# Kernel tuning notes

Measured on AMD Instinct MI355X. Metric: run time of the kernel, lower is better.

The kernel has to match this reference:

```python
import jax, jax.numpy as jnp
import numpy as np

EMBED = 1024
HEADS = 16

def setup_inputs() -> dict:
    key = jax.random.key(0)
    ks = jax.random.split(key, 6)
    N, S = 1, 4096
    half = EMBED // 2
    x = jax.random.normal(ks[0], (N, S, EMBED), dtype=jnp.float32)
    Wq = jax.random.normal(ks[1], (half, half), dtype=jnp.float32) * 0.02
    Wk = jax.random.normal(ks[2], (half, half), dtype=jnp.float32) * 0.02
    Wv = jax.random.normal(ks[3], (half, half), dtype=jnp.float32) * 0.02
    Wo = jax.random.normal(ks[4], (EMBED, half), dtype=jnp.float32) * 0.02
    bo = jnp.zeros((EMBED,), dtype=jnp.float32)
    return {"x": x, "Wq": Wq, "Wk": Wk, "Wv": Wv, "Wo": Wo, "bo": bo}

def reference(x, Wq, Wk, Wv, Wo, bo):
    N, S, E = x.shape
    H = HEADS
    Dh = (E // 2) // H                 # per-head dim of the half-width projections (32)
    scale = float(E // H) ** 0.5       # original scales by head_dim = embed/heads = 64
    left = x[..., : E // 2]            # only the left chunk feeds attention in the source
    # torch Linear: y = x @ W.T (no bias)
    q = (left @ Wq.T).reshape(N, S, H, Dh)
    k = (left @ Wk.T).reshape(N, S, H, Dh)
    v = (left @ Wv.T).reshape(N, S, H, Dh)
    energy = jnp.einsum('nqhd,nkhd->nqkh', q, k)          # [N,S,S,H] full score tensor
    att = jax.nn.softmax(energy / scale, axis=2)          # softmax over key axis
    out = jnp.einsum('nqkh,nkhd->nqhd', att, v)           # [N,S,H,Dh]
    out = out.reshape(N, S, E // 2)
    return out @ Wo.T + bo                                # fc_out: half -> embed
```

## Files before the change

kernel.cpp:

```cpp
#include <hip/hip_runtime.h>
#include <stdint.h>


#define SEQ    4096
#define DMODEL 1024
#define DHALF  512
#define NH     16
#define DH     32

typedef __attribute__((ext_vector_type(4))) float facc4;
typedef __attribute__((ext_vector_type(8))) short bfrag8;

#define MFMA_BF16(a, b, c) __builtin_amdgcn_mfma_f32_16x16x32_bf16((a), (b), (c), 0, 0, 0)

static __device__ __forceinline__ uint16_t f2b(float x) {
    uint32_t u = __float_as_uint(x);
    return (uint16_t)((u + 0x7FFFu + ((u >> 16) & 1u)) >> 16);
}
static __device__ __forceinline__ float b2f(uint16_t b) {
    return __uint_as_float(((uint32_t)b) << 16);
}

static __device__ __forceinline__ bfrag8 cvt8perm(float4 a, float4 b) {
    uint32_t u0 = __float_as_uint(a.x) + 0x8000u, u1 = __float_as_uint(a.y) + 0x8000u;
    uint32_t u2 = __float_as_uint(a.z) + 0x8000u, u3 = __float_as_uint(a.w) + 0x8000u;
    uint32_t u4 = __float_as_uint(b.x) + 0x8000u, u5 = __float_as_uint(b.y) + 0x8000u;
    uint32_t u6 = __float_as_uint(b.z) + 0x8000u, u7 = __float_as_uint(b.w) + 0x8000u;
    union { uint32_t w[4]; bfrag8 r; } u;
    u.w[0] = __builtin_amdgcn_perm(u1, u0, 0x07060302u);
    u.w[1] = __builtin_amdgcn_perm(u3, u2, 0x07060302u);
    u.w[2] = __builtin_amdgcn_perm(u5, u4, 0x07060302u);
    u.w[3] = __builtin_amdgcn_perm(u7, u6, 0x07060302u);
    return u.r;
}

__global__ __launch_bounds__(256) void convert_w(
    const float* __restrict__ Wq, const float* __restrict__ Wk,
    const float* __restrict__ Wv, const float* __restrict__ Wo,
    const float* __restrict__ x,
    uint16_t* __restrict__ q, uint16_t* __restrict__ k,
    uint16_t* __restrict__ v, uint16_t* __restrict__ o,
    uint16_t* __restrict__ xb)
{
    int zz = blockIdx.x;
    if (zz >= 640) {
        size_t g = (size_t)(zz - 640) * 2048 + (size_t)threadIdx.x * 8;
        int row = (int)(g >> 9);
        int col = (int)(g & 511);
        const float* src = &x[(size_t)row * DMODEL + col];
        float4 a = *(const float4*)src;
        float4 b = *(const float4*)(src + 4);
        *(bfrag8*)&xb[g] = cvt8perm(a, b);
        return;
    }
    const float* src; uint16_t* dst; size_t off;
    if      (zz < 128) { src = Wq; dst = q; off = (size_t)zz * 2048; }
    else if (zz < 256) { src = Wk; dst = k; off = (size_t)(zz - 128) * 2048; }
    else if (zz < 384) { src = Wv; dst = v; off = (size_t)(zz - 256) * 2048; }
    else               { src = Wo; dst = o; off = (size_t)(zz - 384) * 2048; }
    size_t i = off + (size_t)threadIdx.x * 8;
    float4 a = *(const float4*)&src[i];
    float4 b = *(const float4*)&src[i + 4];
    *(bfrag8*)&dst[i] = cvt8perm(a, b);
}

__device__ __forceinline__ void gemm128(
    const uint16_t* __restrict__ A, int lda,
    const uint16_t* __restrict__ B, int ldb,
    void* __restrict__ C, int ldc, int cF32,
    const float* __restrict__ bias, float scale,
    int Kd, int m0, int n0)
{
    __shared__ __align__(16) uint16_t As[2][128 * 40];
    __shared__ __align__(16) uint16_t Bs[2][128 * 40];

    const int tid  = threadIdx.x;
    const int lane = tid & 63;
    const int wv   = tid >> 6;
    const int lo   = lane & 15;
    const int quad = lane >> 4;
    const int srow = tid >> 2;
    const int skq  = (tid & 3) * 8;
    const int rb   = (wv >> 1) * 64;
    const int cb   = (wv & 1) * 64;

    const facc4 ZACC = {0.f, 0.f, 0.f, 0.f};
    facc4 acc[4][4];
#pragma unroll
    for (int i = 0; i < 4; ++i)
#pragma unroll
        for (int j = 0; j < 4; ++j) acc[i][j] = ZACC;

    const uint16_t* hA0 = &A[(size_t)(m0 + srow) * lda + skq];
    const uint16_t* hA1 = &A[(size_t)(m0 + srow + 64) * lda + skq];
    const uint16_t* pB0 = &B[(size_t)(n0 + srow) * ldb + skq];
    const uint16_t* pB1 = &B[(size_t)(n0 + srow + 64) * ldb + skq];

    bfrag8 ra0 = *(const bfrag8*)hA0;
    bfrag8 ra1 = *(const bfrag8*)hA1;
    bfrag8 rb0 = *(const bfrag8*)pB0;
    bfrag8 rb1 = *(const bfrag8*)pB1;

    *(bfrag8*)&As[0][srow * 40 + skq]        = ra0;
    *(bfrag8*)&As[0][(srow + 64) * 40 + skq] = ra1;
    *(bfrag8*)&Bs[0][srow * 40 + skq]        = rb0;
    *(bfrag8*)&Bs[0][(srow + 64) * 40 + skq] = rb1;
    __syncthreads();

    int p = 0;
    for (int kt = 0; kt < Kd; kt += 32) {
        const bool more = (kt + 32 < Kd);
        if (more) {
            ra0 = *(const bfrag8*)(hA0 + kt + 32);
            ra1 = *(const bfrag8*)(hA1 + kt + 32);
            rb0 = *(const bfrag8*)(pB0 + kt + 32);
            rb1 = *(const bfrag8*)(pB1 + kt + 32);
        }

        bfrag8 af[4], bf[4];
#pragma unroll
        for (int i = 0; i < 4; ++i) {
            af[i] = *(const bfrag8*)&As[p][(rb + i * 16 + lo) * 40 + quad * 8];
            bf[i] = *(const bfrag8*)&Bs[p][(cb + i * 16 + lo) * 40 + quad * 8];
        }
#pragma unroll
        for (int i = 0; i < 4; ++i)
#pragma unroll
            for (int j = 0; j < 4; ++j)
                acc[i][j] = MFMA_BF16(bf[j], af[i], acc[i][j]);

        if (more) {
            *(bfrag8*)&As[1 - p][srow * 40 + skq]        = ra0;
            *(bfrag8*)&As[1 - p][(srow + 64) * 40 + skq] = ra1;
            *(bfrag8*)&Bs[1 - p][srow * 40 + skq]        = rb0;
            *(bfrag8*)&Bs[1 - p][(srow + 64) * 40 + skq] = rb1;
            __syncthreads();
            p ^= 1;
        }
    }

#pragma unroll
    for (int i = 0; i < 4; ++i) {
        const size_t row = (size_t)(m0 + rb + i * 16 + lo);
#pragma unroll
        for (int j = 0; j < 4; ++j) {
            const int colb = n0 + cb + j * 16 + quad * 4;
            float4 bv = {0.f, 0.f, 0.f, 0.f};
            if (bias) bv = *(const float4*)&bias[colb];
            float v0 = acc[i][j][0] * scale + bv.x;
            float v1 = acc[i][j][1] * scale + bv.y;
            float v2 = acc[i][j][2] * scale + bv.z;
            float v3 = acc[i][j][3] * scale + bv.w;
            if (cF32) {
                float4 o = {v0, v1, v2, v3};
                *(float4*)&((float*)C)[row * ldc + colb] = o;
            } else {
                uint2 o;
                o.x = (uint32_t)f2b(v0) | ((uint32_t)f2b(v1) << 16);
                o.y = (uint32_t)f2b(v2) | ((uint32_t)f2b(v3) << 16);
                *(uint2*)&((uint16_t*)C)[row * ldc + colb] = o;
            }
        }
    }
}

#define SC_Q (0.125f * 1.4426950408889634f)

__global__ __launch_bounds__(256, 2) void qkv_kernel(
    const uint16_t* __restrict__ xb,
    const uint16_t* __restrict__ Wqb, const uint16_t* __restrict__ Wkb,
    const uint16_t* __restrict__ Wvb,
    uint16_t* __restrict__ Q, uint16_t* __restrict__ K, uint16_t* __restrict__ V)
{
    const int z = blockIdx.z;
    const uint16_t* W = (z == 0) ? Wqb : (z == 1) ? Wkb : Wvb;
    uint16_t* Out     = (z == 0) ? Q   : (z == 1) ? K   : V;
    float scale       = (z == 0) ? SC_Q : 1.0f;
    gemm128(xb, DHALF, W, DHALF, Out, DHALF, 0, nullptr, scale, DHALF,
            blockIdx.y * 128, blockIdx.x * 128);
}

__global__ __launch_bounds__(256, 2) void outproj_kernel(
    const uint16_t* __restrict__ O, const uint16_t* __restrict__ Wob,
    const float* __restrict__ bo, float* __restrict__ Y)
{
    gemm128(O, DHALF, Wob, DHALF, Y, DMODEL, 1, bo, 1.0f, DHALF,
            blockIdx.y * 128, blockIdx.x * 128);
}

__global__ __launch_bounds__(512) void attn_kernel(
    const uint16_t* __restrict__ Q, const uint16_t* __restrict__ Kb,
    const uint16_t* __restrict__ Vb, uint16_t* __restrict__ Op,
    float* __restrict__ lbuf, int kspan)
{
    __shared__ __align__(16) uint16_t Ks[2][128 * 40];
    __shared__ __align__(16) uint16_t Vt[2][32 * 128];

    const int tid  = threadIdx.x;
    const int lane = tid & 63;
    const int wv   = tid >> 6;
    const int lo   = lane & 15;
    const int quad = lane >> 4;

    const int f  = blockIdx.x + 16 * blockIdx.y + 256 * blockIdx.z;
    const int pp = (f & 7) | ((f >> 7) << 3);
    const int h  = pp & 15;
    const int sp = pp >> 4;
    const int q0 = ((f >> 3) & 15) * 256;

    const int srow = tid >> 2;
    const int skq  = (tid & 3) * 8;

    const facc4 ZACC = {0.f, 0.f, 0.f, 0.f};

    bfrag8 qf[2];
    qf[0] = *(const bfrag8*)&Q[(size_t)(q0 + wv * 32 + lo) * DHALF + h * DH + quad * 8];
    qf[1] = *(const bfrag8*)&Q[(size_t)(q0 + wv * 32 + 16 + lo) * DHALF + h * DH + quad * 8];

    bfrag8 ones;
#pragma unroll
    for (int j = 0; j < 8; ++j) ones[j] = (short)0x3F80;

    int vt_w[8];
    {
        int pb = ((srow >> 5) << 2) | ((srow >> 2) & 3);
        int pw = (((srow >> 4) & 1) << 2) | (srow & 3);
#pragma unroll
        for (int j = 0; j < 8; ++j) {
            int d  = skq + j;
            int Rd = ((d & 7) + 2 * (d >> 3)) & 7;
            vt_w[j] = d * 128 + (((pb + Rd) & 15) << 3) + pw;
        }
    }
    int vt_r[4][2];
#pragma unroll
    for (int dt = 0; dt < 2; ++dt) {
        int d  = dt * 16 + lo;
        int Rd = ((d & 7) + 2 * (d >> 3)) & 7;
#pragma unroll
        for (int c = 0; c < 4; ++c)
            vt_r[c][dt] = d * 128 + ((((c * 4 + quad) + Rd) & 15) << 3);
    }
    const int ks_r = lo * 40 + quad * 8;

    const uint16_t* kp = &Kb[(size_t)(sp * kspan + srow) * DHALF + h * DH + skq];
    const uint16_t* vp = &Vb[(size_t)(sp * kspan + srow) * DHALF + h * DH + skq];

    facc4 oacc[2][2], oaccL[2];
    oacc[0][0] = ZACC; oacc[0][1] = ZACC;
    oacc[1][0] = ZACC; oacc[1][1] = ZACC;
    oaccL[0] = ZACC; oaccL[1] = ZACC;

    float4 kreg = *(const float4*)kp;
    float4 vreg = *(const float4*)vp;
    kp += 128 * DHALF;
    vp += 128 * DHALF;

#define STAGE(BUF) do {                                                       \
        *(float4*)&Ks[BUF][srow * 40 + skq] = kreg;                           \
        const uint16_t* vsp = (const uint16_t*)&vreg;                         \
        _Pragma("unroll")                                                     \
        for (int j = 0; j < 8; ++j) Vt[BUF][vt_w[j]] = vsp[j];                \
    } while (0)

#define HALF(BUF, HH) do {                                                    \
        uint2 w0[4], w1[4];                                                   \
        _Pragma("unroll")                                                     \
        for (int t4 = 0; t4 < 4; ++t4) {                                      \
            bfrag8 kf = *(const bfrag8*)&Ks[BUF][(4 * HH + t4) * 640 + ks_r]; \
            facc4 s0 = MFMA_BF16(kf, qf[0], ZACC);                            \
            facc4 s1 = MFMA_BF16(kf, qf[1], ZACC);                            \
            uint32_t a0 = __float_as_uint(__builtin_amdgcn_exp2f(s0[0])) + 0x8000u; \
            uint32_t a1 = __float_as_uint(__builtin_amdgcn_exp2f(s0[1])) + 0x8000u; \
            uint32_t a2 = __float_as_uint(__builtin_amdgcn_exp2f(s0[2])) + 0x8000u; \
            uint32_t a3 = __float_as_uint(__builtin_amdgcn_exp2f(s0[3])) + 0x8000u; \
            w0[t4].x = __builtin_amdgcn_perm(a1, a0, 0x07060302u);            \
            w0[t4].y = __builtin_amdgcn_perm(a3, a2, 0x07060302u);            \
            uint32_t b0 = __float_as_uint(__builtin_amdgcn_exp2f(s1[0])) + 0x8000u; \
            uint32_t b1 = __float_as_uint(__builtin_amdgcn_exp2f(s1[1])) + 0x8000u; \
            uint32_t b2 = __float_as_uint(__builtin_amdgcn_exp2f(s1[2])) + 0x8000u; \
            uint32_t b3 = __float_as_uint(__builtin_amdgcn_exp2f(s1[3])) + 0x8000u; \
            w1[t4].x = __builtin_amdgcn_perm(b1, b0, 0x07060302u);            \
            w1[t4].y = __builtin_amdgcn_perm(b3, b2, 0x07060302u);            \
        }                                                                     \
        union PU { uint2 u2[2]; bfrag8 f; } pu;                               \
        bfrag8 pf0[2], pf1[2];                                                \
        pu.u2[0] = w0[0]; pu.u2[1] = w0[1]; pf0[0] = pu.f;                    \
        pu.u2[0] = w0[2]; pu.u2[1] = w0[3]; pf0[1] = pu.f;                    \
        pu.u2[0] = w1[0]; pu.u2[1] = w1[1]; pf1[0] = pu.f;                    \
        pu.u2[0] = w1[2]; pu.u2[1] = w1[3]; pf1[1] = pu.f;                    \
        _Pragma("unroll")                                                     \
        for (int cc = 0; cc < 2; ++cc) {                                      \
            _Pragma("unroll")                                                 \
            for (int dt = 0; dt < 2; ++dt) {                                  \
                bfrag8 vf = *(const bfrag8*)&Vt[BUF][vt_r[2 * HH + cc][dt]];  \
                oacc[0][dt] = MFMA_BF16(pf0[cc], vf, oacc[0][dt]);            \
                oacc[1][dt] = MFMA_BF16(pf1[cc], vf, oacc[1][dt]);            \
            }                                                                 \
            oaccL[0] = MFMA_BF16(pf0[cc], ones, oaccL[0]);                    \
            oaccL[1] = MFMA_BF16(pf1[cc], ones, oaccL[1]);                    \
        }                                                                     \
    } while (0)

#define TILE(BUF) do { HALF(BUF, 0); HALF(BUF, 1); } while (0)

    STAGE(0);
    __syncthreads();

    const int nt = kspan >> 7;
    for (int t = 0; t < nt; t += 2) {
        kreg = *(const float4*)kp;
        vreg = *(const float4*)vp;
        kp += 128 * DHALF; vp += 128 * DHALF;
        TILE(0);
        STAGE(1);
        __syncthreads();

        const bool more = (t + 2 < nt);
        if (more) {
            kreg = *(const float4*)kp;
            vreg = *(const float4*)vp;
            kp += 128 * DHALF; vp += 128 * DHALF;
        }
        TILE(1);
        if (more) {
            STAGE(0);
            __syncthreads();
        }
    }
#undef STAGE
#undef HALF
#undef TILE

    if (lo == 0) {
#pragma unroll
        for (int g = 0; g < 2; ++g)
#pragma unroll
            for (int r = 0; r < 4; ++r)
                lbuf[((size_t)sp * NH + h) * SEQ + q0 + wv * 32 + g * 16 + quad * 4 + r] =
                    oaccL[g][r];
    }

    uint16_t* Od = Op + (size_t)sp * SEQ * DHALF;
#pragma unroll
    for (int g = 0; g < 2; ++g) {
#pragma unroll
        for (int r = 0; r < 4; ++r) {
            int row = q0 + wv * 32 + g * 16 + quad * 4 + r;
            Od[(size_t)row * DHALF + h * DH + lo]      = f2b(oacc[g][0][r]);
            Od[(size_t)row * DHALF + h * DH + 16 + lo] = f2b(oacc[g][1][r]);
        }
    }
}

__global__ __launch_bounds__(256) void combine_kernel(
    const uint16_t* __restrict__ Op, const float* __restrict__ lbuf,
    uint16_t* __restrict__ O, int ns)
{
    int t   = blockIdx.x * 256 + threadIdx.x;
    int row = t >> 6;
    int cb  = (t & 63) << 3;
    int h   = cb >> 5;
    float l = 0.f;
    float acc[8] = {0.f, 0.f, 0.f, 0.f, 0.f, 0.f, 0.f, 0.f};
    for (int sp = 0; sp < ns; ++sp) {
        l += lbuf[((size_t)sp * NH + h) * SEQ + row];
        bfrag8 a = *(const bfrag8*)&Op[(size_t)sp * SEQ * DHALF + (size_t)row * DHALF + cb];
#pragma unroll
        for (int j = 0; j < 8; ++j) acc[j] += b2f((uint16_t)a[j]);
    }
    float inv = 1.0f / l;
    bfrag8 o;
#pragma unroll
    for (int j = 0; j < 8; ++j) o[j] = (short)f2b(acc[j] * inv);
    *(bfrag8*)&O[(size_t)row * DHALF + cb] = o;
}

extern "C" void kernel_launch(void* const* d_in, const int* in_sizes, int n_in,
                              void* d_out, int out_size, void* d_ws, size_t ws_size,
                              hipStream_t stream)
{
    const float* x  = (const float*)d_in[0];
    const float* Wq = (const float*)d_in[1];
    const float* Wk = (const float*)d_in[2];
    const float* Wv = (const float*)d_in[3];
    const float* Wo = (const float*)d_in[4];
    const float* bo = (const float*)d_in[5];

    size_t fixed_e = 3 * (size_t)DHALF * DHALF + (size_t)DMODEL * DHALF
                   + 4 * (size_t)SEQ * DHALF;
    size_t need4 = (fixed_e + 4 * (size_t)SEQ * DHALF) * 2
                 + 4 * (size_t)NH * SEQ * 4;
    const int ns = (ws_size >= need4) ? 4 : 2;

    uint16_t* Wqb = (uint16_t*)d_ws;
    uint16_t* Wkb = Wqb + (size_t)DHALF * DHALF;
    uint16_t* Wvb = Wkb + (size_t)DHALF * DHALF;
    uint16_t* Wob = Wvb + (size_t)DHALF * DHALF;
    uint16_t* Q   = Wob + (size_t)DMODEL * DHALF;
    uint16_t* K   = Q + (size_t)SEQ * DHALF;
    uint16_t* V   = K + (size_t)SEQ * DHALF;
    uint16_t* O   = V + (size_t)SEQ * DHALF;
    uint16_t* Op  = O + (size_t)SEQ * DHALF;
    float*  lbuf  = (float*)(Op + (size_t)ns * SEQ * DHALF);
    uint16_t* xb  = O;

    convert_w<<<1664, 256, 0, stream>>>(Wq, Wk, Wv, Wo, x, Wqb, Wkb, Wvb, Wob, xb);
    qkv_kernel<<<dim3(DHALF / 128, SEQ / 128, 3), 256, 0, stream>>>(
        xb, Wqb, Wkb, Wvb, Q, K, V);
    attn_kernel<<<dim3(SEQ / 256, NH, ns), 512, 0, stream>>>(Q, K, V, Op, lbuf, SEQ / ns);
    combine_kernel<<<1024, 256, 0, stream>>>(Op, lbuf, O, ns);
    outproj_kernel<<<dim3(DMODEL / 128, SEQ / 128), 256, 0, stream>>>(
        O, Wob, bo, (float*)d_out);
}
```

Baseline: 163.5 us.

## Load GEMM tiles directly to LDS with XOR swizzle and fix attention split to 2

The shared GEMM tile loader now uses global_load_lds to copy 16-byte chunks straight from global memory into LDS, replacing the register round-trip. An XOR swizzle on the column offset avoids bank conflicts now that the padded 40-wide rows are gone. Separately, the attention key split is hard-coded to 2 instead of choosing 4 when workspace allows, which halves the parallel attention blocks but shrinks the combine step. The direct-to-LDS path relies on the asynchronous loads being complete at the barrier.

```diff
diff --git a/kernel.cpp b/kernel.cpp
--- a/kernel.cpp
+++ b/kernel.cpp
@@ -12,6 +12,12 @@
 typedef __attribute__((ext_vector_type(8))) short bfrag8;
 
 #define MFMA_BF16(a, b, c) __builtin_amdgcn_mfma_f32_16x16x32_bf16((a), (b), (c), 0, 0, 0)
+
+static __device__ __forceinline__ void gll16(const void* g, void* l) {
+    typedef const __attribute__((address_space(1))) void GV;
+    typedef __attribute__((address_space(3))) void LV;
+    __builtin_amdgcn_global_load_lds((GV*)g, (LV*)l, 16, 0, 0);
+}
 
 static __device__ __forceinline__ uint16_t f2b(float x) {
     uint32_t u = __float_as_uint(x);
@@ -71,16 +77,14 @@
     const float* __restrict__ bias, float scale,
     int Kd, int m0, int n0)
 {
-    __shared__ __align__(16) uint16_t As[2][128 * 40];
-    __shared__ __align__(16) uint16_t Bs[2][128 * 40];
+    __shared__ __align__(16) uint16_t As[2][128 * 32];
+    __shared__ __align__(16) uint16_t Bs[2][128 * 32];
 
     const int tid  = threadIdx.x;
     const int lane = tid & 63;
     const int wv   = tid >> 6;
     const int lo   = lane & 15;
     const int quad = lane >> 4;
-    const int srow = tid >> 2;
-    const int skq  = (tid & 3) * 8;
     const int rb   = (wv >> 1) * 64;
     const int cb   = (wv & 1) * 64;
 
@@ -91,37 +95,34 @@
 #pragma unroll
         for (int j = 0; j < 4; ++j) acc[i][j] = ZACC;
 
-    const uint16_t* hA0 = &A[(size_t)(m0 + srow) * lda + skq];
-    const uint16_t* hA1 = &A[(size_t)(m0 + srow + 64) * lda + skq];
-    const uint16_t* pB0 = &B[(size_t)(n0 + srow) * ldb + skq];
-    const uint16_t* pB1 = &B[(size_t)(n0 + srow + 64) * ldb + skq];
-
-    bfrag8 ra0 = *(const bfrag8*)hA0;
-    bfrag8 ra1 = *(const bfrag8*)hA1;
-    bfrag8 rb0 = *(const bfrag8*)pB0;
-    bfrag8 rb1 = *(const bfrag8*)pB1;
-
-    *(bfrag8*)&As[0][srow * 40 + skq]        = ra0;
-    *(bfrag8*)&As[0][(srow + 64) * 40 + skq] = ra1;
-    *(bfrag8*)&Bs[0][srow * 40 + skq]        = rb0;
-    *(bfrag8*)&Bs[0][(srow + 64) * 40 + skq] = rb1;
+    const int lrow = lane >> 2;
+    const int scol = (((lane & 3) ^ (lrow & 3)) << 3);
+    const uint16_t* gA0 = &A[(size_t)(m0 + wv * 32 + lrow) * lda + scol];
+    const uint16_t* gA1 = gA0 + (size_t)16 * lda;
+    const uint16_t* gB0 = &B[(size_t)(n0 + wv * 32 + lrow) * ldb + scol];
+    const uint16_t* gB1 = gB0 + (size_t)16 * ldb;
+    const int d0 = wv * 1024;
+    const int d1 = d0 + 512;
+
+    const int rdo = lo * 32 + ((quad ^ (lo & 3)) << 3);
+
+    gll16(gA0, &As[0][d0]); gll16(gA1, &As[0][d1]);
+    gll16(gB0, &Bs[0][d0]); gll16(gB1, &Bs[0][d1]);
     __syncthreads();
 
     int p = 0;
     for (int kt = 0; kt < Kd; kt += 32) {
         const bool more = (kt + 32 < Kd);
         if (more) {
-            ra0 = *(const bfrag8*)(hA0 + kt + 32);
-            ra1 = *(const bfrag8*)(hA1 + kt + 32);
-            rb0 = *(const bfrag8*)(pB0 + kt + 32);
-            rb1 = *(const bfrag8*)(pB1 + kt + 32);
+            gll16(gA0 + kt + 32, &As[1 - p][d0]); gll16(gA1 + kt + 32, &As[1 - p][d1]);
+            gll16(gB0 + kt + 32, &Bs[1 - p][d0]); gll16(gB1 + kt + 32, &Bs[1 - p][d1]);
         }
 
         bfrag8 af[4], bf[4];
 #pragma unroll
         for (int i = 0; i < 4; ++i) {
-            af[i] = *(const bfrag8*)&As[p][(rb + i * 16 + lo) * 40 + quad * 8];
-            bf[i] = *(const bfrag8*)&Bs[p][(cb + i * 16 + lo) * 40 + quad * 8];
+            af[i] = *(const bfrag8*)&As[p][rb * 32 + i * 512 + rdo];
+            bf[i] = *(const bfrag8*)&Bs[p][cb * 32 + i * 512 + rdo];
         }
 #pragma unroll
         for (int i = 0; i < 4; ++i)
@@ -130,10 +131,6 @@
                 acc[i][j] = MFMA_BF16(bf[j], af[i], acc[i][j]);
 
         if (more) {
-            *(bfrag8*)&As[1 - p][srow * 40 + skq]        = ra0;
-            *(bfrag8*)&As[1 - p][(srow + 64) * 40 + skq] = ra1;
-            *(bfrag8*)&Bs[1 - p][srow * 40 + skq]        = rb0;
-            *(bfrag8*)&Bs[1 - p][(srow + 64) * 40 + skq] = rb1;
             __syncthreads();
             p ^= 1;
         }
@@ -387,11 +384,7 @@
     const float* Wo = (const float*)d_in[4];
     const float* bo = (const float*)d_in[5];
 
-    size_t fixed_e = 3 * (size_t)DHALF * DHALF + (size_t)DMODEL * DHALF
-                   + 4 * (size_t)SEQ * DHALF;
-    size_t need4 = (fixed_e + 4 * (size_t)SEQ * DHALF) * 2
-                 + 4 * (size_t)NH * SEQ * 4;
-    const int ns = (ws_size >= need4) ? 4 : 2;
+    const int ns = 2;
 
     uint16_t* Wqb = (uint16_t*)d_ws;
     uint16_t* Wkb = Wqb + (size_t)DHALF * DHALF;
```

Result: no change. 161.0 us (-1.5%).
